# Kernel optimization log

Hardware: AMD Instinct MI355X
Metric: run time of the kernel (lower is better)

## Reference

```python
import jax, jax.numpy as jnp
import numpy as np

NUM_HEADS = 8
EPS = 1e-12  # torch F.normalize eps


def _l2norm(t):
    n = jnp.linalg.norm(t, axis=-1, keepdims=True)
    return t / jnp.maximum(n, EPS)


def setup_inputs() -> dict:
    key = jax.random.key(0)
    k1, k2, k3 = jax.random.split(key, 3)
    B, T, N, D = 16, 12, 1024, 128
    x = jax.random.normal(k1, (B, T, N, D), dtype=jnp.float32)
    # Linear(model_dim, 3*model_dim, bias=False): stored as (D, 3D) for x @ W
    W_qkv = jax.random.normal(k2, (D, 3 * D), dtype=jnp.float32) * (1.0 / np.sqrt(D))
    W_out = jax.random.normal(k3, (D, D), dtype=jnp.float32) * (1.0 / np.sqrt(D))
    b_out = jnp.zeros((D,), dtype=jnp.float32)
    return {"x": x, "W_qkv": W_qkv, "W_out": W_out, "b_out": b_out}


def reference(x, W_qkv, W_out, b_out):
    B, T, N, D = x.shape
    H = NUM_HEADS
    hd = D // H
    qkv = x @ W_qkv                                  # (B,T,N,3D)
    q, k, v = jnp.split(qkv, 3, axis=-1)
    # split heads + flatten (B,T) -> b = B*T, matching torch stack/flatten
    qs = _l2norm(q.reshape(B * T, N, H, hd))          # (b,N,H,m)
    ks = _l2norm(k.reshape(B * T, N, H, hd))
    vs = v.reshape(B * T, N, H, hd)
    # linear attention: running kv sum + normalizer
    kvs = jnp.einsum('blhm,blhd->bhmd', ks, vs)       # (b,H,m,d)
    attn_num = jnp.einsum('bnhm,bhmd->bnhd', qs, kvs) + N * vs
    ks_sum = jnp.sum(ks, axis=1)                      # (b,H,m)
    normalizer = jnp.einsum('bnhm,bhm->bnh', qs, ks_sum)[..., None] + N
    out = attn_num / normalizer                       # (b,N,H,d)
    out = out.reshape(B, T, N, D)
    return out @ W_out + b_out
```

## Files before the change

kernel.cpp:

```cpp
#include <hip/hip_runtime.h>

#define NBATCH 192
#define SEQ    1024
#define DIM    128
#define NH     8
#define EPS    1e-12f

typedef short bf16x8 __attribute__((ext_vector_type(8)));
typedef float f32x4  __attribute__((ext_vector_type(4)));

#define KVS_F  393216
#define ZERO_F 417792

static __device__ __forceinline__ unsigned short f2bf(float f) {
    unsigned u = __builtin_bit_cast(unsigned, f);
    u += 0x7fff + ((u >> 16) & 1);
    return (unsigned short)(u >> 16);
}

template <int CTRL>
static __device__ __forceinline__ float dpp_add(float v) {
    int j = __builtin_amdgcn_mov_dpp(__builtin_bit_cast(int, v), CTRL, 0xf, 0xf, false);
    return v + __builtin_bit_cast(float, j);
}
static __device__ __forceinline__ float r16sum(float v) {
    v = dpp_add<0xB1>(v);
    v = dpp_add<0x4E>(v);
    v = dpp_add<0x141>(v);
    v = dpp_add<0x140>(v);
    return v;
}

static __device__ __forceinline__ int strip_addr(int row, int el) {
    return row * 32 + ((((el >> 3) ^ (row & 3)) << 3) | (el & 7));
}

static __device__ __forceinline__ uint2 pack4(float a, float b, float c, float d) {
    uint2 r;
    r.x = (unsigned)f2bf(a) | ((unsigned)f2bf(b) << 16);
    r.y = (unsigned)f2bf(c) | ((unsigned)f2bf(d) << 16);
    return r;
}

static __device__ __forceinline__ bf16x8 cvt8(float4 a, float4 b) {
    bf16x8 r;
    r[0] = (short)f2bf(a.x); r[1] = (short)f2bf(a.y); r[2] = (short)f2bf(a.z); r[3] = (short)f2bf(a.w);
    r[4] = (short)f2bf(b.x); r[5] = (short)f2bf(b.y); r[6] = (short)f2bf(b.z); r[7] = (short)f2bf(b.w);
    return r;
}

static __device__ __forceinline__ bf16x8 gfrag(const unsigned short* __restrict__ wT,
                                               int ct, int ks, int lane) {
    return *reinterpret_cast<const bf16x8*>(wT + ((ct * 4 + ks) * 64 + lane) * 8);
}

__global__ __launch_bounds__(256) void k0_prep(const float* __restrict__ Wqkv,
                                               const float* __restrict__ Wout,
                                               unsigned short* __restrict__ wsWT) {
    int i = blockIdx.x * 256 + threadIdx.x;
    int which = i >> 14, e = i & 16383;
    int j = e & 7, f = e >> 3;
    int n15 = f & 15, q = (f >> 4) & 3, ks = (f >> 6) & 3, ct = f >> 8;
    int k = ks * 32 + q * 8 + j, n = ct * 16 + n15;
    float v = (which < 3) ? Wqkv[k * 384 + which * 128 + n] : Wout[k * 128 + n];
    wsWT[i] = f2bf(v);
}

__global__ __launch_bounds__(512, 4) void k1_kv(const float* __restrict__ x,
                                                const unsigned short* __restrict__ wsWT,
                                                float* __restrict__ kvs_ws,
                                                float* __restrict__ kssum_ws) {
    __shared__ float redf[16384];
    unsigned short* strips = reinterpret_cast<unsigned short*>(redf);
    int t = threadIdx.x, w = t >> 6, lane = t & 63, q = lane >> 4, n15 = lane & 15;
    int b = blockIdx.x >> 2, seg = blockIdx.x & 3;
    const unsigned short* wkT = wsWT + 16384;
    const unsigned short* wvT = wsWT + 32768;
    unsigned short* knS = strips + w * 1024;
    unsigned short* vS  = knS + 512;

    bf16x8 ah[2][4];
#pragma unroll
    for (int rs = 0; rs < 2; ++rs) {
        int row = seg * 256 + w * 32 + rs * 16 + n15;
        const float* xr = x + (size_t)(b * SEQ + row) * DIM;
#pragma unroll
        for (int ks = 0; ks < 4; ++ks) {
            float4 p0 = *reinterpret_cast<const float4*>(xr + ks * 32 + q * 8);
            float4 p1 = *reinterpret_cast<const float4*>(xr + ks * 32 + q * 8 + 4);
            ah[rs][ks] = cvt8(p0, p1);
        }
    }

    f32x4 kvsacc[8];
    float ksum[8];
#pragma unroll
    for (int h = 0; h < 8; ++h) { kvsacc[h] = (f32x4){0,0,0,0}; ksum[h] = 0.f; }

#pragma unroll
    for (int ct = 0; ct < 8; ++ct) {
        f32x4 ka[2] = {(f32x4){0,0,0,0}, (f32x4){0,0,0,0}};
        f32x4 va[2] = {(f32x4){0,0,0,0}, (f32x4){0,0,0,0}};
#pragma unroll
        for (int ks = 0; ks < 4; ++ks) {
            bf16x8 kb = gfrag(wkT, ct, ks, lane);
            bf16x8 vb = gfrag(wvT, ct, ks, lane);
#pragma unroll
            for (int rs = 0; rs < 2; ++rs) {
                ka[rs] = __builtin_amdgcn_mfma_f32_16x16x32_bf16(ah[rs][ks], kb, ka[rs], 0, 0, 0);
                va[rs] = __builtin_amdgcn_mfma_f32_16x16x32_bf16(ah[rs][ks], vb, va[rs], 0, 0, 0);
            }
        }
#pragma unroll
        for (int rs = 0; rs < 2; ++rs) {
            float kn[4];
#pragma unroll
            for (int r = 0; r < 4; ++r) {
                float val = ka[rs][r];
                float ssq = r16sum(val * val);
                float di  = 1.0f / fmaxf(sqrtf(ssq), EPS);
                kn[r] = val * di;
                ksum[ct] += kn[r];
            }
            *reinterpret_cast<uint2*>(knS + strip_addr(n15, rs * 16 + q * 4)) =
                pack4(kn[0], kn[1], kn[2], kn[3]);
            *reinterpret_cast<uint2*>(vS + strip_addr(n15, rs * 16 + q * 4)) =
                pack4(va[rs][0], va[rs][1], va[rs][2], va[rs][3]);
        }
        bf16x8 aK = *reinterpret_cast<const bf16x8*>(knS + strip_addr(n15, q * 8));
        bf16x8 bV = *reinterpret_cast<const bf16x8*>(vS + strip_addr(n15, q * 8));
        kvsacc[ct] = __builtin_amdgcn_mfma_f32_16x16x32_bf16(aK, bV, kvsacc[ct], 0, 0, 0);
    }

#pragma unroll
    for (int ct = 0; ct < 8; ++ct) {
        float s = ksum[ct];
        s += __shfl_xor(s, 16); s += __shfl_xor(s, 32);
        if (lane < 16) atomicAdd(&kssum_ws[b * 128 + ct * 16 + n15], s);
    }

    __syncthreads();
#pragma unroll
    for (int ct = 0; ct < 8; ++ct)
#pragma unroll
        for (int r = 0; r < 4; ++r)
            redf[w * 2048 + ct * 256 + (q * 4 + r) * 16 + n15] = kvsacc[ct][r];
    __syncthreads();
#pragma unroll
    for (int i = 0; i < 4; ++i) {
        int el = i * 512 + t;
        float s = 0.f;
#pragma unroll
        for (int ww = 0; ww < 8; ++ww) s += redf[ww * 2048 + el];
        atomicAdd(&kvs_ws[b * 2048 + el], s);
    }
}

__global__ __launch_bounds__(512, 4) void k2_out(const float* __restrict__ x,
                                                 const unsigned short* __restrict__ wsWT,
                                                 const float* __restrict__ kvs_ws,
                                                 const float* __restrict__ kssum_ws,
                                                 const float* __restrict__ bout,
                                                 float* __restrict__ out) {
    __shared__ unsigned short lds[40960];
    unsigned short* kvsT   = lds;
    unsigned short* strips = lds + 4096;
    unsigned short* tile   = lds + 8192;
    int t = threadIdx.x, w = t >> 6, lane = t & 63, q = lane >> 4, n15 = lane & 15;
    int b = blockIdx.x >> 2, seg = blockIdx.x & 3, rowbase = seg * 256;
    const unsigned short* wqT = wsWT;
    const unsigned short* wvT = wsWT + 32768;
    const unsigned short* woT = wsWT + 49152;

    {
        int row = t >> 2, part = t & 3, h = row >> 4, d = row & 15;
        unsigned es[8];
#pragma unroll
        for (int j = 0; j < 8; j += 2) {
            int m0 = part * 8 + j;
            unsigned lo = (m0     < 16) ? f2bf(kvs_ws[b * 2048 + h * 256 + m0 * 16 + d])      : 0;
            unsigned hi = (m0 + 1 < 16) ? f2bf(kvs_ws[b * 2048 + h * 256 + (m0 + 1) * 16 + d]) : 0;
            es[j] = lo | (hi << 16);
        }
        uint4 v = {es[0], es[2], es[4], es[6]};
        *reinterpret_cast<uint4*>(kvsT + row * 32 + ((part ^ (row & 3)) << 3)) = v;
    }

    float kss[8];
#pragma unroll
    for (int h = 0; h < 8; ++h) kss[h] = kssum_ws[b * 128 + h * 16 + n15];

    bf16x8 ah[2][4];
#pragma unroll
    for (int rs = 0; rs < 2; ++rs) {
        int row = rowbase + w * 32 + rs * 16 + n15;
        const float* xr = x + (size_t)(b * SEQ + row) * DIM;
#pragma unroll
        for (int ks = 0; ks < 4; ++ks) {
            float4 p0 = *reinterpret_cast<const float4*>(xr + ks * 32 + q * 8);
            float4 p1 = *reinterpret_cast<const float4*>(xr + ks * 32 + q * 8 + 4);
            ah[rs][ks] = cvt8(p0, p1);
        }
    }

    unsigned short* myS = strips + w * 512;
    unsigned short* tw  = tile + w * 4096;
    {
        uint2 z = {0, 0};
        *reinterpret_cast<uint2*>(myS + strip_addr(n15, 16 + q * 4)) = z;
    }
    __syncthreads();

#pragma unroll
    for (int rs = 0; rs < 2; ++rs)
#pragma unroll
        for (int h = 0; h < 8; ++h) {
            f32x4 qa = (f32x4){0,0,0,0};
            f32x4 va = (f32x4){0,0,0,0};
#pragma unroll
            for (int ks = 0; ks < 4; ++ks) {
                bf16x8 qb = gfrag(wqT, h, ks, lane);
                bf16x8 vb = gfrag(wvT, h, ks, lane);
                qa = __builtin_amdgcn_mfma_f32_16x16x32_bf16(ah[rs][ks], qb, qa, 0, 0, 0);
                va = __builtin_amdgcn_mfma_f32_16x16x32_bf16(ah[rs][ks], vb, va, 0, 0, 0);
            }
            float pv[4];
#pragma unroll
            for (int r = 0; r < 4; ++r) {
                float val = qa[r];
                float ssq = r16sum(val * val);
                float tt  = r16sum(val * kss[h]);
                float di  = 1.0f / fmaxf(sqrtf(ssq), EPS);
                float inv = 1.0f / (tt * di + (float)SEQ);
                pv[r] = val * di * inv;
                va[r] *= (float)SEQ * inv;
            }
#pragma unroll
            for (int r = 0; r < 4; ++r)
                myS[strip_addr(q * 4 + r, n15)] = f2bf(pv[r]);
            bf16x8 aq = *reinterpret_cast<const bf16x8*>(myS + strip_addr(n15, q * 8));
            bf16x8 bk = *reinterpret_cast<const bf16x8*>(kvsT + strip_addr(h * 16 + n15, q * 8));
            va = __builtin_amdgcn_mfma_f32_16x16x32_bf16(aq, bk, va, 0, 0, 0);
#pragma unroll
            for (int r = 0; r < 4; ++r) {
                int rt = rs * 16 + q * 4 + r;
                int colg = h * 2 + (n15 >> 3);
                tw[rt * 128 + (((colg ^ (rt & 15)) << 3) | (n15 & 7))] = f2bf(va[r]);
            }
        }

    bf16x8 ap[2][4];
#pragma unroll
    for (int rs = 0; rs < 2; ++rs)
#pragma unroll
        for (int ks = 0; ks < 4; ++ks) {
            int rt = rs * 16 + n15;
            ap[rs][ks] = *reinterpret_cast<const bf16x8*>(
                tw + rt * 128 + ((((ks << 2) + q) ^ (rt & 15)) << 3));
        }
#pragma unroll
    for (int ct = 0; ct < 8; ++ct) {
        f32x4 o0 = (f32x4){0,0,0,0};
        f32x4 o1 = (f32x4){0,0,0,0};
#pragma unroll
        for (int ks = 0; ks < 4; ++ks) {
            bf16x8 bb = gfrag(woT, ct, ks, lane);
            o0 = __builtin_amdgcn_mfma_f32_16x16x32_bf16(ap[0][ks], bb, o0, 0, 0, 0);
            o1 = __builtin_amdgcn_mfma_f32_16x16x32_bf16(ap[1][ks], bb, o1, 0, 0, 0);
        }
        float bo = bout[ct * 16 + n15];
#pragma unroll
        for (int r = 0; r < 4; ++r) {
            int row0 = rowbase + w * 32 + q * 4 + r;
            out[(size_t)(b * SEQ + row0) * DIM + ct * 16 + n15]      = o0[r] + bo;
            out[(size_t)(b * SEQ + row0 + 16) * DIM + ct * 16 + n15] = o1[r] + bo;
        }
    }
}

extern "C" void kernel_launch(void* const* d_in, const int* in_sizes, int n_in,
                              void* d_out, int out_size, void* d_ws, size_t ws_size,
                              hipStream_t stream) {
    const float* x    = (const float*)d_in[0];
    const float* Wqkv = (const float*)d_in[1];
    const float* Wout = (const float*)d_in[2];
    const float* bout = (const float*)d_in[3];
    float* out = (float*)d_out;

    float* kvs_ws   = (float*)d_ws;
    float* kssum_ws = kvs_ws + KVS_F;
    unsigned short* wsWT = (unsigned short*)((char*)d_ws + (size_t)ZERO_F * 4);

    hipMemsetAsync(d_ws, 0, (size_t)ZERO_F * 4, stream);
    k0_prep<<<dim3(256), dim3(256), 0, stream>>>(Wqkv, Wout, wsWT);
    k1_kv<<<dim3(768), dim3(512), 0, stream>>>(x, wsWT, kvs_ws, kssum_ws);
    k2_out<<<dim3(768), dim3(512), 0, stream>>>(x, wsWT, kvs_ws, kssum_ws, bout, out);
}
```

Measured before the change: 316.9 us.

## Cut register pressure by rolling loops and storing per-iteration kv partials to LDS

```diff
diff --git a/kernel.cpp b/kernel.cpp
--- a/kernel.cpp
+++ b/kernel.cpp
@@ -71,7 +71,7 @@
                                                 float* __restrict__ kvs_ws,
                                                 float* __restrict__ kssum_ws) {
     __shared__ float redf[16384];
-    unsigned short* strips = reinterpret_cast<unsigned short*>(redf);
+    __shared__ unsigned short strips[8192];
     int t = threadIdx.x, w = t >> 6, lane = t & 63, q = lane >> 4, n15 = lane & 15;
     int b = blockIdx.x >> 2, seg = blockIdx.x & 3;
     const unsigned short* wkT = wsWT + 16384;
@@ -92,12 +92,7 @@
         }
     }
 
-    f32x4 kvsacc[8];
-    float ksum[8];
-#pragma unroll
-    for (int h = 0; h < 8; ++h) { kvsacc[h] = (f32x4){0,0,0,0}; ksum[h] = 0.f; }
-
-#pragma unroll
+#pragma unroll 1
     for (int ct = 0; ct < 8; ++ct) {
         f32x4 ka[2] = {(f32x4){0,0,0,0}, (f32x4){0,0,0,0}};
         f32x4 va[2] = {(f32x4){0,0,0,0}, (f32x4){0,0,0,0}};
@@ -111,6 +106,7 @@
                 va[rs] = __builtin_amdgcn_mfma_f32_16x16x32_bf16(ah[rs][ks], vb, va[rs], 0, 0, 0);
             }
         }
+        float ksum = 0.f;
 #pragma unroll
         for (int rs = 0; rs < 2; ++rs) {
             float kn[4];
@@ -120,7 +116,7 @@
                 float ssq = r16sum(val * val);
                 float di  = 1.0f / fmaxf(sqrtf(ssq), EPS);
                 kn[r] = val * di;
-                ksum[ct] += kn[r];
+                ksum += kn[r];
             }
             *reinterpret_cast<uint2*>(knS + strip_addr(n15, rs * 16 + q * 4)) =
                 pack4(kn[0], kn[1], kn[2], kn[3]);
@@ -129,22 +125,15 @@
         }
         bf16x8 aK = *reinterpret_cast<const bf16x8*>(knS + strip_addr(n15, q * 8));
         bf16x8 bV = *reinterpret_cast<const bf16x8*>(vS + strip_addr(n15, q * 8));
-        kvsacc[ct] = __builtin_amdgcn_mfma_f32_16x16x32_bf16(aK, bV, kvsacc[ct], 0, 0, 0);
-    }
-
-#pragma unroll
-    for (int ct = 0; ct < 8; ++ct) {
-        float s = ksum[ct];
+        f32x4 kacc = __builtin_amdgcn_mfma_f32_16x16x32_bf16(aK, bV, (f32x4){0,0,0,0}, 0, 0, 0);
+#pragma unroll
+        for (int r = 0; r < 4; ++r)
+            redf[w * 2048 + ct * 256 + (q * 4 + r) * 16 + n15] = kacc[r];
+        float s = ksum;
         s += __shfl_xor(s, 16); s += __shfl_xor(s, 32);
         if (lane < 16) atomicAdd(&kssum_ws[b * 128 + ct * 16 + n15], s);
     }
 
-    __syncthreads();
-#pragma unroll
-    for (int ct = 0; ct < 8; ++ct)
-#pragma unroll
-        for (int r = 0; r < 4; ++r)
-            redf[w * 2048 + ct * 256 + (q * 4 + r) * 16 + n15] = kvsacc[ct][r];
     __syncthreads();
 #pragma unroll
     for (int i = 0; i < 4; ++i) {
@@ -186,10 +175,6 @@
         *reinterpret_cast<uint4*>(kvsT + row * 32 + ((part ^ (row & 3)) << 3)) = v;
     }
 
-    float kss[8];
-#pragma unroll
-    for (int h = 0; h < 8; ++h) kss[h] = kssum_ws[b * 128 + h * 16 + n15];
-
     bf16x8 ah[2][4];
 #pragma unroll
     for (int rs = 0; rs < 2; ++rs) {
@@ -213,8 +198,9 @@
 
 #pragma unroll
     for (int rs = 0; rs < 2; ++rs)
-#pragma unroll
+#pragma unroll 1
         for (int h = 0; h < 8; ++h) {
+            float kssh = kssum_ws[b * 128 + h * 16 + n15];
             f32x4 qa = (f32x4){0,0,0,0};
             f32x4 va = (f32x4){0,0,0,0};
 #pragma unroll
@@ -229,7 +215,7 @@
             for (int r = 0; r < 4; ++r) {
                 float val = qa[r];
                 float ssq = r16sum(val * val);
-                float tt  = r16sum(val * kss[h]);
+                float tt  = r16sum(val * kssh);
                 float di  = 1.0f / fmaxf(sqrtf(ssq), EPS);
                 float inv = 1.0f / (tt * di + (float)SEQ);
                 pv[r] = val * di * inv;
@@ -258,7 +244,7 @@
             ap[rs][ks] = *reinterpret_cast<const bf16x8*>(
                 tw + rt * 128 + ((((ks << 2) + q) ^ (rt & 15)) << 3));
         }
-#pragma unroll
+#pragma unroll 1
     for (int ct = 0; ct < 8; ++ct) {
         f32x4 o0 = (f32x4){0,0,0,0};
         f32x4 o1 = (f32x4){0,0,0,0};
```

After: 282.2 us. 11.0% less time.
